# Optimization experiments

Measured on AMD Instinct MI355X. Metric: run time of the kernel, lower is better.

Reference implementation:

```python
import jax, jax.numpy as jnp
import numpy as np

SR = 44100  # sample_rate from __init__


def setup_inputs() -> dict:
    key = jax.random.key(0)
    k1, k2 = jax.random.split(key)
    x = jax.random.normal(k1, (64, 2, 131072), dtype=jnp.float32) * 0.1
    t = jax.random.uniform(k2, (64,), dtype=jnp.float32)
    filter_freq = jnp.array([1000.0], dtype=jnp.float32)  # learnable param
    filter_q = jnp.array([0.707], dtype=jnp.float32)      # learnable param
    return {"x": x, "t": t, "filter_freq": filter_freq, "filter_q": filter_q}


def _highpass_biquad(x, filter_freq, filter_q):
    # parameter clamping as in the module's forward
    freq = jnp.clip(filter_freq, 100.0, SR / 2.0 - 1.0)[0]
    q = jnp.clip(filter_q, 0.1, 10.0)[0]
    # torchaudio highpass_biquad coefficients
    w0 = 2.0 * jnp.pi * freq / SR
    cosw = jnp.cos(w0)
    alpha = jnp.sin(w0) / (2.0 * q)
    a0 = 1.0 + alpha
    b0 = ((1.0 + cosw) * 0.5) / a0
    b1 = (-(1.0 + cosw)) / a0
    b2 = b0
    a1 = (-2.0 * cosw) / a0
    a2 = (1.0 - alpha) / a0
    # FIR (feedforward) part, zero initial conditions: fused elementwise
    x1 = jnp.pad(x, ((0, 0), (0, 0), (1, 0)))[..., :-1]
    x2 = jnp.pad(x, ((0, 0), (0, 0), (2, 0)))[..., :-2]
    xf = b0 * x + b1 * x1 + b2 * x2  # [B, C, T]
    # IIR (feedback) 2nd-order recurrence over time, vectorized over (B, C)
    xf_t = jnp.moveaxis(xf, -1, 0)  # [T, B, C]

    def step(carry, u):
        y1, y2 = carry
        y = u - a1 * y1 - a2 * y2
        return (y, y1), y

    zero = jnp.zeros(xf_t.shape[1:], xf_t.dtype)
    _, ys = jax.lax.scan(step, (zero, zero), xf_t)
    y = jnp.moveaxis(ys, 0, -1)  # [B, C, T]
    # torchaudio lfilter default clamp=True
    return jnp.clip(y, -1.0, 1.0)


def reference(x, t, filter_freq, filter_q):
    # t is accepted but unused, matching the original forward signature
    return _highpass_biquad(x, filter_freq, filter_q)
```

## Files before the change

### kernel.cpp

```cpp
#include <hip/hip_runtime.h>
#include <math.h>


constexpr int T_LEN  = 131072;
constexpr int L       = 64;
constexpr int CPB     = 64;
constexpr int SEG     = CPB * L;
constexpr int BLK_PER_SEQ = T_LEN / SEG;
constexpr int NSEQ    = 64 * 2;
constexpr int NBLOCKS = NSEQ * BLK_PER_SEQ;
constexpr int RSTRIDE = L + 1;
constexpr int ROWS    = CPB + 1;

typedef float fx4 __attribute__((ext_vector_type(4)));

__global__ __launch_bounds__(64) void hp_kernel(
    const float* __restrict__ x,
    const float* __restrict__ pfreq,
    const float* __restrict__ pq,
    float* __restrict__ out)
{
    __shared__ float lds[ROWS * RSTRIDE];

    float freq = fminf(fmaxf(pfreq[0], 100.0f), 44100.0f * 0.5f - 1.0f);
    float q    = fminf(fmaxf(pq[0], 0.1f), 10.0f);
    float w0   = 2.0f * (float)M_PI * freq / 44100.0f;
    float cw   = cosf(w0);
    float alpha = sinf(w0) / (2.0f * q);
    float ia0  = 1.0f / (1.0f + alpha);
    const float b0 = (1.0f + cw) * 0.5f * ia0;
    const float b1 = -(1.0f + cw) * ia0;
    const float b2 = b0;
    const float a1 = -2.0f * cw * ia0;
    const float a2 = (1.0f - alpha) * ia0;

    const int b   = blockIdx.x;
    const int seq = b >> 5;
    const int S   = (b & (BLK_PER_SEQ - 1)) * SEG;
    const float* __restrict__ xs = x   + (size_t)seq * T_LEN;
    float*       __restrict__ os = out + (size_t)seq * T_LEN;
    const int tid = threadIdx.x;

    {
        const fx4* gb = (const fx4*)(xs + S - L);
#pragma unroll
        for (int k = 0; k <= 16; ++k) {
            int f = tid + (k << 6);
            if (f < ROWS * (L / 4)) {
                const fx4* sp = (S == 0 && f < 16) ? ((const fx4*)xs + f) : (gb + f);
                fx4 v = *sp;
                int r = f >> 4, p = (f & 15) << 2;
                float* d = &lds[r * RSTRIDE + p];
                d[0] = v.x; d[1] = v.y; d[2] = v.z; d[3] = v.w;
            }
        }
    }
    __syncthreads();

    float y1 = 0.f, y2 = 0.f, p1 = 0.f, p2 = 0.f;

#define STEP(xv, yv) { \
        float xf_ = fmaf(b2, p2, fmaf(b1, p1, b0 * (xv))); \
        yv = fmaf(-a1, y1, fmaf(-a2, y2, xf_)); \
        p2 = p1; p1 = (xv); y2 = y1; y1 = yv; }

    const int cg = (S >> 6) + tid;
    if (cg > 0) {
        if (cg >= 2) {
            if (tid >= 1) {
                p2 = lds[(tid - 1) * RSTRIDE + 62];
                p1 = lds[(tid - 1) * RSTRIDE + 63];
            } else {
                p1 = xs[S - 65];
                p2 = xs[S - 66];
            }
        }
        const float* wr = &lds[tid * RSTRIDE];
#pragma unroll
        for (int j = 0; j < L; ++j) { float u; STEP(wr[j], u); (void)u; }
    }

    {
        float* mr = &lds[(tid + 1) * RSTRIDE];
#pragma unroll
        for (int j = 0; j < L; ++j) {
            float v = mr[j], yy;
            STEP(v, yy);
            mr[j] = fminf(fmaxf(yy, -1.f), 1.f);
        }
    }
    __syncthreads();

    {
        fx4* ob = (fx4*)(os + S);
#pragma unroll
        for (int k = 0; k < 16; ++k) {
            int f = tid + (k << 6);
            int r = (f >> 4) + 1, p = (f & 15) << 2;
            const float* s = &lds[r * RSTRIDE + p];
            fx4 v;
            v.x = s[0]; v.y = s[1]; v.z = s[2]; v.w = s[3];
            ob[f] = v;
        }
    }
#undef STEP
}

extern "C" void kernel_launch(void* const* d_in, const int* in_sizes, int n_in,
                              void* d_out, int out_size, void* d_ws, size_t ws_size,
                              hipStream_t stream) {
    const float* x  = (const float*)d_in[0];
    const float* ff = (const float*)d_in[2];
    const float* fq = (const float*)d_in[3];
    float* out = (float*)d_out;
    hp_kernel<<<NBLOCKS, CPB, 0, stream>>>(x, ff, fq, out);
}
```

Measured before the change: 126.4 us.

## Use XOR-swizzled fx4 LDS layout with direct global-to-LDS loads

Replaces the padded scalar LDS layout (stride L+1) with an fx4 array whose 16-byte chunks are XOR-swizzled per row, so each thread's row accesses avoid bank conflicts while reads and writes stay vectorized. The segment is staged with global_load_lds, bypassing registers, and thread 0 fetches the previous segment's warm-up window straight from global memory into registers instead of an extra LDS row. This cuts LDS instruction count and the scalar ds_read/ds_write traffic. It adds per-thread swizzle index arithmetic and relies on the global_load_lds builtin behaving as assumed for the async copy and its synchronization.

```diff
diff --git a/kernel.cpp b/kernel.cpp
--- a/kernel.cpp
+++ b/kernel.cpp
@@ -9,10 +9,11 @@
 constexpr int BLK_PER_SEQ = T_LEN / SEG;
 constexpr int NSEQ    = 64 * 2;
 constexpr int NBLOCKS = NSEQ * BLK_PER_SEQ;
-constexpr int RSTRIDE = L + 1;
-constexpr int ROWS    = CPB + 1;
 
 typedef float fx4 __attribute__((ext_vector_type(4)));
+
+#define AS1(p) ((const __attribute__((address_space(1))) void*)(p))
+#define AS3(p) ((__attribute__((address_space(3))) void*)(p))
 
 __global__ __launch_bounds__(64) void hp_kernel(
     const float* __restrict__ x,
@@ -20,7 +21,7 @@
     const float* __restrict__ pq,
     float* __restrict__ out)
 {
-    __shared__ float lds[ROWS * RSTRIDE];
+    __shared__ fx4 lds4[CPB * 16];
 
     float freq = fminf(fmaxf(pfreq[0], 100.0f), 44100.0f * 0.5f - 1.0f);
     float q    = fminf(fmaxf(pq[0], 0.1f), 10.0f);
@@ -42,51 +43,67 @@
     const int tid = threadIdx.x;
 
     {
-        const fx4* gb = (const fx4*)(xs + S - L);
+        const float* gseg = xs + S;
 #pragma unroll
-        for (int k = 0; k <= 16; ++k) {
-            int f = tid + (k << 6);
-            if (f < ROWS * (L / 4)) {
-                const fx4* sp = (S == 0 && f < 16) ? ((const fx4*)xs + f) : (gb + f);
-                fx4 v = *sp;
-                int r = f >> 4, p = (f & 15) << 2;
-                float* d = &lds[r * RSTRIDE + p];
-                d[0] = v.x; d[1] = v.y; d[2] = v.z; d[3] = v.w;
-            }
+        for (int k = 0; k < 16; ++k) {
+            int s = tid + (k << 6);
+            int r = s >> 4;
+            int g = (r << 4) | ((s & 15) ^ (r & 15));
+            __builtin_amdgcn_global_load_lds(AS1(gseg + (g << 2)),
+                                             AS3(lds4 + (k << 6)), 16, 0, 0);
         }
     }
+
+    fx4 h[16];
+    if (tid == 0 && S > 0) {
+        const fx4* gw = (const fx4*)(xs + S - L);
+#pragma unroll
+        for (int k = 0; k < 16; ++k) h[k] = gw[k];
+    }
+
     __syncthreads();
 
     float y1 = 0.f, y2 = 0.f, p1 = 0.f, p2 = 0.f;
 
-#define STEP(xv, yv) { \
+#define STEP(xv) { \
         float xf_ = fmaf(b2, p2, fmaf(b1, p1, b0 * (xv))); \
-        yv = fmaf(-a1, y1, fmaf(-a2, y2, xf_)); \
+        float yv  = fmaf(-a1, y1, fmaf(-a2, y2, xf_)); \
         p2 = p1; p1 = (xv); y2 = y1; y1 = yv; }
 
-    const int cg = (S >> 6) + tid;
-    if (cg > 0) {
-        if (cg >= 2) {
-            if (tid >= 1) {
-                p2 = lds[(tid - 1) * RSTRIDE + 62];
-                p1 = lds[(tid - 1) * RSTRIDE + 63];
+    const int cgm = (S >> 6) + tid;
+    if (cgm >= 1) {
+        if (cgm >= 2) {
+            if (tid >= 2) {
+                int rr = tid - 2;
+                const float* pr = (const float*)(lds4 + ((rr << 4) | (15 ^ (rr & 15))));
+                p2 = pr[2]; p1 = pr[3];
             } else {
-                p1 = xs[S - 65];
-                p2 = xs[S - 66];
+                const float* w = xs + S + (tid - 1) * L;
+                p1 = w[-1]; p2 = w[-2];
             }
         }
-        const float* wr = &lds[tid * RSTRIDE];
+        const fx4* rp = lds4 + (((tid - 1) & 63) << 4);
+        const int  xr = (tid - 1) & 15;
 #pragma unroll
-        for (int j = 0; j < L; ++j) { float u; STEP(wr[j], u); (void)u; }
+        for (int j4 = 0; j4 < 16; ++j4) {
+            fx4 v = (tid == 0) ? h[j4] : rp[j4 ^ xr];
+            STEP(v.x); STEP(v.y); STEP(v.z); STEP(v.w);
+        }
     }
 
     {
-        float* mr = &lds[(tid + 1) * RSTRIDE];
+        fx4* mrow = lds4 + (tid << 4);
+        const int xm = tid & 15;
 #pragma unroll
-        for (int j = 0; j < L; ++j) {
-            float v = mr[j], yy;
-            STEP(v, yy);
-            mr[j] = fminf(fmaxf(yy, -1.f), 1.f);
+        for (int j4 = 0; j4 < 16; ++j4) {
+            int idx = j4 ^ xm;
+            fx4 v = mrow[idx];
+            fx4 o;
+            STEP(v.x); o.x = fminf(fmaxf(y1, -1.f), 1.f);
+            STEP(v.y); o.y = fminf(fmaxf(y1, -1.f), 1.f);
+            STEP(v.z); o.z = fminf(fmaxf(y1, -1.f), 1.f);
+            STEP(v.w); o.w = fminf(fmaxf(y1, -1.f), 1.f);
+            mrow[idx] = o;
         }
     }
     __syncthreads();
@@ -96,11 +113,8 @@
 #pragma unroll
         for (int k = 0; k < 16; ++k) {
             int f = tid + (k << 6);
-            int r = (f >> 4) + 1, p = (f & 15) << 2;
-            const float* s = &lds[r * RSTRIDE + p];
-            fx4 v;
-            v.x = s[0]; v.y = s[1]; v.z = s[2]; v.w = s[3];
-            ob[f] = v;
+            int r = f >> 4;
+            ob[f] = lds4[(r << 4) | ((f & 15) ^ (r & 15))];
         }
     }
 #undef STEP
```

Result: faster. 118.4 us (-6.3%).
